# Performance work log

Hardware: AMD Instinct MI355X
Metric: run time of the kernel (lower is better)

Reference implementation:

```python
import jax, jax.numpy as jnp
import numpy as np

N = 10000      # nodes
E = 320000     # edges
F_IN = 33      # input node features
H = 32         # hidden
G = 64         # graphs in batch


def setup_inputs() -> dict:
    key = jax.random.key(0)
    ks = jax.random.split(key, 24)
    s = 0.1  # small init scale for numerical sanity
    inp = {
        "x": jax.random.normal(ks[0], (N, F_IN), jnp.float32),
        "edge_index": jax.random.randint(ks[1], (2, E), 0, N, jnp.int32),
        "edge_attr": jax.random.uniform(ks[2], (E, 1), jnp.float32),
        "batch": jnp.sort(jax.random.randint(ks[3], (N,), 0, G, jnp.int32)),
        # conv1: edge-MLP Linear(1 -> F_IN*H), root weight [F_IN,H], bias [H]
        "nn_w1": jax.random.normal(ks[4], (1, F_IN * H), jnp.float32) * s,
        "nn_b1": jax.random.normal(ks[5], (F_IN * H,), jnp.float32) * s,
        "root1": jax.random.normal(ks[6], (F_IN, H), jnp.float32) * s,
        "bias1": jnp.zeros((H,), jnp.float32),
        # conv2: edge-MLP Linear(1 -> H*H)
        "nn_w2": jax.random.normal(ks[7], (1, H * H), jnp.float32) * s,
        "nn_b2": jax.random.normal(ks[8], (H * H,), jnp.float32) * s,
        "root2": jax.random.normal(ks[9], (H, H), jnp.float32) * s,
        "bias2": jnp.zeros((H,), jnp.float32),
        # conv3
        "nn_w3": jax.random.normal(ks[10], (1, H * H), jnp.float32) * s,
        "nn_b3": jax.random.normal(ks[11], (H * H,), jnp.float32) * s,
        "root3": jax.random.normal(ks[12], (H, H), jnp.float32) * s,
        "bias3": jnp.zeros((H,), jnp.float32),
        # readout MLP: Linear(3H -> H), Linear(H -> 2)
        "lin1_w": jax.random.normal(ks[13], (3 * H, H), jnp.float32) * s,
        "lin1_b": jnp.zeros((H,), jnp.float32),
        "lin2_w": jax.random.normal(ks[14], (H, 2), jnp.float32) * s,
        "lin2_b": jnp.zeros((2,), jnp.float32),
    }
    return inp


def _nnconv(x, src, dst, edge_attr, nn_w, nn_b, root, bias):
    """PyG NNConv (aggr='add'): out_i = x_i @ root + bias + sum_{e: dst(e)=i} x_{src(e)} @ Theta(e_attr)."""
    in_dim, out_dim = root.shape
    # per-edge weight matrix from edge MLP: [E, in, out]
    W = (edge_attr @ nn_w + nn_b).reshape(-1, in_dim, out_dim)
    msg = jnp.einsum('ei,eio->eo', x[src], W)          # gather + per-edge small matmul
    agg = jax.ops.segment_sum(msg, dst, num_segments=N)  # scatter-add into targets
    return agg + x @ root + bias


def reference(x, edge_index, edge_attr, batch,
              nn_w1, nn_b1, root1, bias1,
              nn_w2, nn_b2, root2, bias2,
              nn_w3, nn_b3, root3, bias3,
              lin1_w, lin1_b, lin2_w, lin2_b):
    src, dst = edge_index[0], edge_index[1]
    h = jax.nn.relu(_nnconv(x, src, dst, edge_attr, nn_w1, nn_b1, root1, bias1))
    h = jax.nn.relu(_nnconv(h, src, dst, edge_attr, nn_w2, nn_b2, root2, bias2))
    h = jax.nn.relu(_nnconv(h, src, dst, edge_attr, nn_w3, nn_b3, root3, bias3))
    # global add / mean / max pooling over graphs
    add_p = jax.ops.segment_sum(h, batch, num_segments=G)
    cnt = jax.ops.segment_sum(jnp.ones((N, 1), h.dtype), batch, num_segments=G)
    mean_p = add_p / jnp.maximum(cnt, 1.0)
    max_p = jax.ops.segment_max(h, batch, num_segments=G)
    max_p = jnp.where(jnp.isfinite(max_p), max_p, 0.0)  # guard empty segments
    g = jnp.concatenate([add_p, mean_p, max_p], axis=1)  # [G, 3H]
    g = jax.nn.relu(g @ lin1_w + lin1_b)
    # dropout p=0.5 is identity in eval mode
    logits = g @ lin2_w + lin2_b
    return jax.nn.log_softmax(logits, axis=-1)
```

## Files before the change

kernel.cpp:

```cpp
#include <hip/hip_runtime.h>

constexpr int N_  = 10000;
constexpr int E_  = 320000;
constexpr int F1  = 33;
constexpr int H   = 32;
constexpr int G   = 64;
constexpr int CAP = 96;

constexpr int GRID = 1250;
constexpr int BT   = 256;

__device__ __forceinline__ unsigned bf16r(float x) {
    unsigned u = __float_as_uint(x);
    return (u + 0x7FFFu + ((u >> 16) & 1u)) >> 16;
}

struct Prm {
    const float* x; const int* ei; const float* ea; const int* batch;
    const float* A1; const float* B1; const float* R1; const float* z1;
    const float* A2; const float* B2; const float* R2; const float* z2;
    const float* A3; const float* B3; const float* R3; const float* z3;
    const float* l1w; const float* l1b; const float* l2w; const float* l2b;
    int* counts; int* startsP; unsigned* meta;
    unsigned* UVa; float* Ra; unsigned* UVb; float* Rb; float* Hs;
    float* out;
};

__global__ __launch_bounds__(BT, 5) void k_build(Prm p) {
    const int tid = threadIdx.x, bid = blockIdx.x;
    {
        int e = bid * BT + tid;
        int s = p.ei[e];
        int d = p.ei[E_ + e];
        float av = p.ea[e];
        int pos = atomicAdd(&p.counts[d], 1);
        p.meta[(size_t)d * CAP + pos] = (unsigned)s | (bf16r(av) << 16);
    }
    const int grp = tid >> 5, f = tid & 31;
    const int node = bid * 8 + grp;
    if (f == 0) {
        int b = p.batch[node];
        int bp = (node == 0) ? -1 : p.batch[node - 1];
        if (b != bp) p.startsP[b] = node + 1;
    }
    float u = 0.f, v = 0.f, r = p.z1[f];
    const float* xr = p.x + (size_t)node * F1;
    #pragma unroll
    for (int k = 0; k < F1; ++k) {
        float xv = xr[k];
        u = fmaf(xv, p.A1[k * H + f], u);
        v = fmaf(xv, p.B1[k * H + f], v);
        r = fmaf(xv, p.R1[k * H + f], r);
    }
    p.UVa[(node << 5) | f] = bf16r(u) | (bf16r(v) << 16);
    p.Ra [(node << 5) | f] = r;
}

template<int LAYER>
__global__ __launch_bounds__(BT, 5) void k_agg(Prm p) {
    __shared__ float wL[3][H * H];
    const int tid = threadIdx.x;

    const unsigned* UVin; const float* Rin; unsigned* UVout; float* Rout;
    if (LAYER == 1)      { UVin = p.UVa; Rin = p.Ra; UVout = p.UVb; Rout = p.Rb; }
    else if (LAYER == 2) { UVin = p.UVb; Rin = p.Rb; UVout = p.UVa; Rout = p.Ra; }
    else                 { UVin = p.UVa; Rin = p.Ra; UVout = nullptr; Rout = nullptr; }

    if (LAYER == 1) {
        for (int i = tid; i < H * H; i += BT) {
            wL[0][i] = p.A2[i]; wL[1][i] = p.B2[i]; wL[2][i] = p.R2[i];
        }
    } else if (LAYER == 2) {
        for (int i = tid; i < H * H; i += BT) {
            wL[0][i] = p.A3[i]; wL[1][i] = p.B3[i]; wL[2][i] = p.R3[i];
        }
    }
    if (LAYER < 3) __syncthreads();

    const int lane = tid & 63, wav = tid >> 6;
    const int f = lane & 31;
    const float zf = (LAYER == 1) ? p.z2[f] : (LAYER == 2) ? p.z3[f] : 0.f;

    const int n = blockIdx.x * 8 + wav * 2 + (lane >> 5);
    const int dg = p.counts[n];
    const unsigned* mrow = p.meta + (size_t)n * CAP;
    unsigned m0 = mrow[f], m1 = mrow[32 + f], m2 = mrow[64 + f];
    float r = Rin[(n << 5) | f];

    float acc = 0.f;
    unsigned mvA[16], wA[16], mvB[16], wB[16];

    auto issue = [&](unsigned (&mv)[16], unsigned (&w)[16], unsigned mreg, int jb) {
        #pragma unroll
        for (int i = 0; i < 16; ++i) {
            mv[i] = __shfl(mreg, (lane & 32) | ((jb + i) & 31), 64);
            unsigned src = min(mv[i] & 0xFFFFu, (unsigned)(N_ - 1));
            w[i] = UVin[(src << 5) | f];
        }
    };
    auto consume = [&](unsigned (&mv)[16], unsigned (&w)[16], int jb) {
        #pragma unroll
        for (int i = 0; i < 16; ++i) {
            float tv = fmaf(__uint_as_float(mv[i] & 0xFFFF0000u),
                            __uint_as_float(w[i] << 16),
                            __uint_as_float(w[i] & 0xFFFF0000u));
            if (jb + i < dg) acc += tv;
        }
    };

    issue(mvA, wA, m0, 0);
    issue(mvB, wB, m0, 16);
    consume(mvA, wA, 0);
    issue(mvA, wA, m1, 32);
    consume(mvB, wB, 16);
    const bool t48 = __any(dg > 48);
    if (t48) issue(mvB, wB, m1, 48);
    consume(mvA, wA, 32);
    if (t48) {
        consume(mvB, wB, 48);
        if (__any(dg > 64)) {
            issue(mvA, wA, m2, 64);
            issue(mvB, wB, m2, 80);
            consume(mvA, wA, 64);
            consume(mvB, wB, 80);
        }
    }

    float h = fmaxf(r + acc, 0.f);

    if (LAYER == 3) {
        p.Hs[(n << 5) | f] = h;
    } else {
        float u = 0.f, v = 0.f, rn = zf;
        #pragma unroll
        for (int k = 0; k < H; ++k) {
            float hk = __shfl(h, k, 32);
            u  = fmaf(hk, wL[0][k * H + f], u);
            v  = fmaf(hk, wL[1][k * H + f], v);
            rn = fmaf(hk, wL[2][k * H + f], rn);
        }
        UVout[(n << 5) | f] = bf16r(u) | (bf16r(v) << 16);
        Rout [(n << 5) | f] = rn;
    }
}

__global__ __launch_bounds__(BT, 5) void k_pool(Prm p) {
    __shared__ int   sst[G];
    __shared__ float gpl[3 * H];
    const int tid = threadIdx.x;
    const int g = blockIdx.x;
    if (tid < G) sst[tid] = p.startsP[tid];
    __syncthreads();
    int sp = sst[g];
    int s0 = 0, e0 = 0;
    if (sp != 0) {
        s0 = sp - 1;
        e0 = N_;
        for (int j = g + 1; j < G; ++j)
            if (sst[j]) { e0 = sst[j] - 1; break; }
    }
    int f = tid >> 3, oct = tid & 7;
    float sum = 0.f, mx = 0.f;
    for (int n = s0 + oct; n < e0; n += 8) {
        float w = p.Hs[(n << 5) | f];
        sum += w;
        mx = fmaxf(mx, w);
    }
    sum += __shfl_xor(sum, 1); mx = fmaxf(mx, __shfl_xor(mx, 1));
    sum += __shfl_xor(sum, 2); mx = fmaxf(mx, __shfl_xor(mx, 2));
    sum += __shfl_xor(sum, 4); mx = fmaxf(mx, __shfl_xor(mx, 4));
    if (oct == 0) {
        float c = fmaxf((float)(e0 - s0), 1.0f);
        gpl[f] = sum;
        gpl[H + f] = sum / c;
        gpl[2 * H + f] = mx;
    }
    __syncthreads();
    if (tid < 32) {
        float hacc = p.l1b[tid];
        #pragma unroll
        for (int k = 0; k < H; ++k) {
            hacc = fmaf(gpl[k],         p.l1w[k * H + tid], hacc);
            hacc = fmaf(gpl[H + k],     p.l1w[(H + k) * H + tid], hacc);
            hacc = fmaf(gpl[2 * H + k], p.l1w[(2 * H + k) * H + tid], hacc);
        }
        float hid = fmaxf(hacc, 0.f);
        float p0 = hid * p.l2w[tid * 2 + 0];
        float p1 = hid * p.l2w[tid * 2 + 1];
        #pragma unroll
        for (int o = 16; o; o >>= 1) {
            p0 += __shfl_xor(p0, o, 32);
            p1 += __shfl_xor(p1, o, 32);
        }
        if (tid == 0) {
            float l0 = p0 + p.l2b[0], l1 = p1 + p.l2b[1];
            float m = fmaxf(l0, l1);
            float lse = m + logf(expf(l0 - m) + expf(l1 - m));
            p.out[g * 2 + 0] = l0 - lse;
            p.out[g * 2 + 1] = l1 - lse;
        }
    }
}


extern "C" void kernel_launch(void* const* d_in, const int* in_sizes, int n_in,
                              void* d_out, int out_size, void* d_ws, size_t ws_size,
                              hipStream_t stream) {
    const float* x      = (const float*)d_in[0];
    const int*   ei     = (const int*)  d_in[1];
    const float* ea     = (const float*)d_in[2];
    const int*   batch  = (const int*)  d_in[3];
    const float* nn_w1  = (const float*)d_in[4];
    const float* nn_b1  = (const float*)d_in[5];
    const float* root1  = (const float*)d_in[6];
    const float* bias1  = (const float*)d_in[7];
    const float* nn_w2  = (const float*)d_in[8];
    const float* nn_b2  = (const float*)d_in[9];
    const float* root2  = (const float*)d_in[10];
    const float* bias2  = (const float*)d_in[11];
    const float* nn_w3  = (const float*)d_in[12];
    const float* nn_b3  = (const float*)d_in[13];
    const float* root3  = (const float*)d_in[14];
    const float* bias3  = (const float*)d_in[15];
    const float* lin1_w = (const float*)d_in[16];
    const float* lin1_b = (const float*)d_in[17];
    const float* lin2_w = (const float*)d_in[18];
    const float* lin2_b = (const float*)d_in[19];
    float* out = (float*)d_out;

    char* ws = (char*)d_ws;
    size_t off = 0;
    auto alloc = [&](size_t bytes) -> void* {
        void* p = ws + off;
        off += (bytes + 255) & ~(size_t)255;
        return p;
    };
    const size_t zbytes = N_ * sizeof(int) + G * sizeof(int);
    char* zchunk = (char*)alloc(zbytes);
    int* counts  = (int*)zchunk;
    int* startsP = (int*)(zchunk + N_ * sizeof(int));
    unsigned* meta = (unsigned*)alloc((size_t)N_ * CAP * sizeof(unsigned));
    unsigned* UVa = (unsigned*)alloc((size_t)N_ * H * sizeof(unsigned));
    float*    Ra  = (float*)   alloc((size_t)N_ * H * sizeof(float));
    unsigned* UVb = (unsigned*)alloc((size_t)N_ * H * sizeof(unsigned));
    float*    Rb  = (float*)   alloc((size_t)N_ * H * sizeof(float));
    float*    Hs  = (float*)   alloc((size_t)N_ * H * sizeof(float));

    Prm prm{ x, ei, ea, batch,
             nn_w1, nn_b1, root1, bias1,
             nn_w2, nn_b2, root2, bias2,
             nn_w3, nn_b3, root3, bias3,
             lin1_w, lin1_b, lin2_w, lin2_b,
             counts, startsP, meta, UVa, Ra, UVb, Rb, Hs, out };

    hipMemsetAsync(zchunk, 0, zbytes, stream);
    k_build <<<GRID, BT, 0, stream>>>(prm);
    k_agg<1><<<GRID, BT, 0, stream>>>(prm);
    k_agg<2><<<GRID, BT, 0, stream>>>(prm);
    k_agg<3><<<GRID, BT, 0, stream>>>(prm);
    k_pool  <<<G,    BT, 0, stream>>>(prm);
}
```

Before: 165.9 us.

## Gather neighbor features as 16-byte vectors with four edges per lane group

The aggregation loop now has each lane load a uint4 (four packed bf16 feature pairs) per edge, so four edge rows are gathered at once by 8-lane groups instead of one 4-byte load per lane per edge. Partial sums are reduced across the lane groups with xor shuffles and then redistributed to per-feature lanes. The goal is fewer, wider memory instructions and more loads in flight through a 6-slot software pipeline. The cost is extra shuffles for the reduction and redistribution, plus different register pressure.

```diff
diff --git a/kernel.cpp b/kernel.cpp
--- a/kernel.cpp
+++ b/kernel.cpp
@@ -78,69 +78,87 @@
     if (LAYER < 3) __syncthreads();
 
     const int lane = tid & 63, wav = tid >> 6;
-    const int f = lane & 31;
-    const float zf = (LAYER == 1) ? p.z2[f] : (LAYER == 2) ? p.z3[f] : 0.f;
-
+    const int l2 = lane & 31;
+    const int rg = l2 >> 3;
+    const int fq = l2 & 7;
     const int n = blockIdx.x * 8 + wav * 2 + (lane >> 5);
     const int dg = p.counts[n];
     const unsigned* mrow = p.meta + (size_t)n * CAP;
-    unsigned m0 = mrow[f], m1 = mrow[32 + f], m2 = mrow[64 + f];
-    float r = Rin[(n << 5) | f];
-
-    float acc = 0.f;
-    unsigned mvA[16], wA[16], mvB[16], wB[16];
-
-    auto issue = [&](unsigned (&mv)[16], unsigned (&w)[16], unsigned mreg, int jb) {
-        #pragma unroll
-        for (int i = 0; i < 16; ++i) {
-            mv[i] = __shfl(mreg, (lane & 32) | ((jb + i) & 31), 64);
-            unsigned src = min(mv[i] & 0xFFFFu, (unsigned)(N_ - 1));
-            w[i] = UVin[(src << 5) | f];
-        }
+    unsigned m0 = mrow[l2], m1 = mrow[32 + l2], m2 = mrow[64 + l2];
+    float r = Rin[(n << 5) | l2];
+
+    float a0 = 0.f, a1 = 0.f, a2 = 0.f, a3 = 0.f;
+    uint4 wq[6]; unsigned mq[6];
+
+    auto issue = [&](unsigned mreg, int t, int sl) {
+        int j = 4 * t + rg;
+        unsigned mv = __shfl(mreg, (lane & 32) | (j & 31), 64);
+        mq[sl] = mv;
+        unsigned src = min(mv & 0xFFFFu, (unsigned)(N_ - 1));
+        wq[sl] = *reinterpret_cast<const uint4*>(UVin + ((size_t)src << 5) + 4 * fq);
     };
-    auto consume = [&](unsigned (&mv)[16], unsigned (&w)[16], int jb) {
-        #pragma unroll
-        for (int i = 0; i < 16; ++i) {
-            float tv = fmaf(__uint_as_float(mv[i] & 0xFFFF0000u),
-                            __uint_as_float(w[i] << 16),
-                            __uint_as_float(w[i] & 0xFFFF0000u));
-            if (jb + i < dg) acc += tv;
-        }
+    auto use = [&](int t, int sl) {
+        unsigned mv = mq[sl]; uint4 w = wq[sl];
+        float a = __uint_as_float(mv & 0xFFFF0000u);
+        bool live = (4 * t + rg) < dg;
+        float t0 = fmaf(a, __uint_as_float(w.x << 16), __uint_as_float(w.x & 0xFFFF0000u));
+        float t1 = fmaf(a, __uint_as_float(w.y << 16), __uint_as_float(w.y & 0xFFFF0000u));
+        float t2 = fmaf(a, __uint_as_float(w.z << 16), __uint_as_float(w.z & 0xFFFF0000u));
+        float t3 = fmaf(a, __uint_as_float(w.w << 16), __uint_as_float(w.w & 0xFFFF0000u));
+        if (live) { a0 += t0; a1 += t1; a2 += t2; a3 += t3; }
     };
 
-    issue(mvA, wA, m0, 0);
-    issue(mvB, wB, m0, 16);
-    consume(mvA, wA, 0);
-    issue(mvA, wA, m1, 32);
-    consume(mvB, wB, 16);
-    const bool t48 = __any(dg > 48);
-    if (t48) issue(mvB, wB, m1, 48);
-    consume(mvA, wA, 32);
-    if (t48) {
-        consume(mvB, wB, 48);
+    issue(m0, 0, 0); issue(m0, 1, 1); issue(m0, 2, 2);
+    issue(m0, 3, 3); issue(m0, 4, 4); issue(m0, 5, 5);
+    #pragma unroll
+    for (int t = 0; t < 12; ++t) {
+        use(t, t % 6);
+        if (t + 6 < 12) issue((t + 6 <= 7) ? m0 : m1, t + 6, t % 6);
+    }
+    if (__any(dg > 48)) {
+        #pragma unroll
+        for (int t = 12; t < 16; ++t) issue(m1, t, t - 12);
+        #pragma unroll
+        for (int t = 12; t < 16; ++t) use(t, t - 12);
         if (__any(dg > 64)) {
-            issue(mvA, wA, m2, 64);
-            issue(mvB, wB, m2, 80);
-            consume(mvA, wA, 64);
-            consume(mvB, wB, 80);
-        }
-    }
-
-    float h = fmaxf(r + acc, 0.f);
+            #pragma unroll
+            for (int t = 16; t < 20; ++t) issue(m2, t, t - 16);
+            #pragma unroll
+            for (int t = 16; t < 20; ++t) use(t, t - 16);
+            #pragma unroll
+            for (int t = 20; t < 24; ++t) issue(m2, t, t - 20);
+            #pragma unroll
+            for (int t = 20; t < 24; ++t) use(t, t - 20);
+        }
+    }
+
+    a0 += __shfl_xor(a0, 8);  a0 += __shfl_xor(a0, 16);
+    a1 += __shfl_xor(a1, 8);  a1 += __shfl_xor(a1, 16);
+    a2 += __shfl_xor(a2, 8);  a2 += __shfl_xor(a2, 16);
+    a3 += __shfl_xor(a3, 8);  a3 += __shfl_xor(a3, 16);
+
+    int rsrc = (lane & 32) | (l2 >> 2);
+    float s0 = __shfl(a0, rsrc, 64), s1 = __shfl(a1, rsrc, 64);
+    float s2 = __shfl(a2, rsrc, 64), s3 = __shfl(a3, rsrc, 64);
+    int c = l2 & 3;
+    float accf = (c == 0) ? s0 : (c == 1) ? s1 : (c == 2) ? s2 : s3;
+
+    float h = fmaxf(r + accf, 0.f);
 
     if (LAYER == 3) {
-        p.Hs[(n << 5) | f] = h;
+        p.Hs[(n << 5) | l2] = h;
     } else {
+        const float zf = (LAYER == 1) ? p.z2[l2] : p.z3[l2];
         float u = 0.f, v = 0.f, rn = zf;
         #pragma unroll
         for (int k = 0; k < H; ++k) {
             float hk = __shfl(h, k, 32);
-            u  = fmaf(hk, wL[0][k * H + f], u);
-            v  = fmaf(hk, wL[1][k * H + f], v);
-            rn = fmaf(hk, wL[2][k * H + f], rn);
-        }
-        UVout[(n << 5) | f] = bf16r(u) | (bf16r(v) << 16);
-        Rout [(n << 5) | f] = rn;
+            u  = fmaf(hk, wL[0][k * H + l2], u);
+            v  = fmaf(hk, wL[1][k * H + l2], v);
+            rn = fmaf(hk, wL[2][k * H + l2], rn);
+        }
+        UVout[(n << 5) | l2] = bf16r(u) | (bf16r(v) << 16);
+        Rout [(n << 5) | l2] = rn;
     }
 }
 
```

Result: faster. 159.5 us (-3.9%).
